# Kernel tuning notes

Measured on AMD Instinct MI355X. Metric: run time of the kernel, lower is better.

Reference implementation:

```python
import jax, jax.numpy as jnp
import numpy as np

N, K, D, E, H, O = 8192, 16, 256, 128, 512, 256


def _mlp(v, W1, W2):
    # nn.Sequential(Linear(no bias), Tanh, Linear(no bias)) with torch [out,in] weights
    return jnp.tanh(v @ W1.T) @ W2.T


def setup_inputs() -> dict:
    key = jax.random.key(0)
    ks = jax.random.split(key, 16)
    def rn(k, shape, s=1.0):
        return jax.random.normal(k, shape, jnp.float32) * s
    return {
        "x": rn(ks[0], (N, D)),
        "neibs": rn(ks[1], (N * K, D)),
        "edge_emb": rn(ks[2], (N * K, E)),
        "mask": jax.random.randint(ks[3], (N, K), 0, 2, jnp.int32),
        "W1x": rn(ks[4], (H, D), 0.02), "W2x": rn(ks[5], (H, H), 0.02),
        "W1n": rn(ks[6], (H, D), 0.02), "W2n": rn(ks[7], (H, H), 0.02),
        "W1e": rn(ks[8], (H, E), 0.02), "W2e": rn(ks[9], (H, H), 0.02),
        "Wfx": rn(ks[10], (O, D), 0.02), "bfx": jnp.zeros((O,), jnp.float32),
        "Wfn": rn(ks[11], (O, D), 0.02), "bfn": jnp.zeros((O,), jnp.float32),
        "Wfe": rn(ks[12], (O, E), 0.02), "bfe": jnp.zeros((O,), jnp.float32),
    }


def reference(x, neibs, edge_emb, mask, W1x, W2x, W1n, W2n, W1e, W2e,
              Wfx, bfx, Wfn, bfn, Wfe, bfe):
    n, d = x.shape
    e = edge_emb.shape[1]
    x_att = _mlp(x, W1x, W2x)                                  # [N,H]
    neib_att = _mlp(neibs, W1n, W2n).reshape(n, -1, H)         # [N,K,H]
    edge_att = _mlp(edge_emb, W1e, W2e).reshape(n, -1, H)      # [N,K,H]

    # node-neighbor attention (scaled by hard-coded sqrt(512))
    ws = jnp.einsum('nkh,nh->nk', neib_att, x_att) / np.sqrt(512.0).astype(np.float32)
    ws = jax.nn.softmax(ws, axis=1)
    agg_neib = jnp.einsum('nk,nkd->nd', ws, neibs.reshape(n, -1, d))
    out = jnp.concatenate([x @ Wfx.T + bfx, agg_neib @ Wfn.T + bfn], axis=1)

    # node-edge attention (unscaled, masked)
    ws2 = jnp.einsum('nkh,nh->nk', edge_att, x_att)
    ws2 = ws2 + (-9999999.0) * mask.astype(x.dtype)
    ws2 = jax.nn.softmax(ws2, axis=1)
    agg_edge = jnp.einsum('nk,nke->ne', ws2, edge_emb.reshape(n, -1, e))
    out = jnp.concatenate([out, agg_edge @ Wfe.T + bfe], axis=1)  # [N,3*O]
    return jax.nn.relu(out)
```

## Files before the change

### kernel.cpp

```cpp
#include <hip/hip_runtime.h>
#include <hip/hip_bf16.h>

typedef __bf16 bf16;
typedef __bf16 bf16x2 __attribute__((ext_vector_type(2)));
typedef __bf16 bf16x4 __attribute__((ext_vector_type(4)));
typedef __bf16 bf16x8 __attribute__((ext_vector_type(8)));
typedef float  f32x4  __attribute__((ext_vector_type(4)));

__device__ __forceinline__ void async16(const bf16* g, bf16* l) {
  __builtin_amdgcn_global_load_lds(
      (__attribute__((address_space(1))) void*)g,
      (__attribute__((address_space(3))) void*)l,
      16, 0, 0);
}

__device__ __forceinline__ void fence_barrier() {
  asm volatile("s_waitcnt vmcnt(0) lgkmcnt(0)" ::: "memory");
  __syncthreads();
}

__device__ __forceinline__ float fast_tanh(float x) {
  float e = __builtin_amdgcn_exp2f(x * 2.88539008177793f);
  return 1.f - 2.f * __builtin_amdgcn_rcpf(e + 1.f);
}

__device__ __forceinline__ int swz(int elem, int row) {
  return elem ^ ((row & 7) << 3);
}

template<int ACT, typename OT>
__global__ __launch_bounds__(256, 4)
void gemm64(const bf16* __restrict__ A, const bf16* __restrict__ W,
            OT* __restrict__ C, int K, int ldc, float alpha,
            const float* __restrict__ bias) {
  __shared__ bf16 As[64 * 64];
  __shared__ bf16 Bs[64 * 64];
  const int tid  = threadIdx.x;
  const int wave = tid >> 6, lane = tid & 63;
  const int wr = wave >> 1, wc = wave & 1;
  const int g = lane >> 4, l4 = lane & 15;

  f32x4 acc[2][2];
#pragma unroll
  for (int i = 0; i < 2; ++i)
#pragma unroll
    for (int j = 0; j < 2; ++j)
      acc[i][j] = (f32x4){0.f, 0.f, 0.f, 0.f};

  const bf16* Abase = A + (size_t)blockIdx.x * 64 * K;
  const bf16* Wbase = W + (size_t)blockIdx.y * 64 * K;

  for (int k0 = 0; k0 < K; k0 += 64) {
#pragma unroll
    for (int i = 0; i < 2; ++i) {
      const int cb  = i * 256 + wave * 64;
      const int c   = cb + lane;
      const int row = c >> 3;
      const int kk  = ((c & 7) ^ (row & 7)) << 3;
      async16(Abase + (size_t)row * K + k0 + kk, &As[cb * 8]);
      async16(Wbase + (size_t)row * K + k0 + kk, &Bs[cb * 8]);
    }
    fence_barrier();
#pragma unroll
    for (int s = 0; s < 2; ++s) {
      const int koff = s * 32 + g * 8;
      bf16x8 af[2], bfr[2];
#pragma unroll
      for (int i = 0; i < 2; ++i) {
        const int ra = wr * 32 + i * 16 + l4;
        af[i] = *(const bf16x8*)&As[ra * 64 + swz(koff, ra)];
      }
#pragma unroll
      for (int j = 0; j < 2; ++j) {
        const int rb = wc * 32 + j * 16 + l4;
        bfr[j] = *(const bf16x8*)&Bs[rb * 64 + swz(koff, rb)];
      }
#pragma unroll
      for (int i = 0; i < 2; ++i)
#pragma unroll
        for (int j = 0; j < 2; ++j)
          acc[i][j] = __builtin_amdgcn_mfma_f32_16x16x32_bf16(af[i], bfr[j], acc[i][j], 0, 0, 0);
    }
    fence_barrier();
  }

  const int rbase = blockIdx.x * 64 + wr * 32;
  const int cbase = blockIdx.y * 64 + wc * 32;
#pragma unroll
  for (int i = 0; i < 2; ++i)
#pragma unroll
    for (int j = 0; j < 2; ++j) {
      const int col = cbase + j * 16 + l4;
      const float bv = bias ? bias[col] : 0.f;
#pragma unroll
      for (int r = 0; r < 4; ++r) {
        const int row = rbase + i * 16 + g * 4 + r;
        float v = acc[i][j][r] * alpha + bv;
        if (ACT == 1) v = fast_tanh(v);
        if (ACT == 2) v = fmaxf(v, 0.f);
        C[(size_t)row * ldc + col] = (OT)v;
      }
    }
}

template<int D>
__global__ __launch_bounds__(256, 2)
void score_agg(const float* __restrict__ A, const bf16* __restrict__ Wb,
               const bf16* __restrict__ y, int ldy, int yoff, float scale,
               const int* __restrict__ mask, bf16* __restrict__ agg) {
  __shared__ bf16 As[64 * D];
  __shared__ bf16 Bs[256 * 64];
  float* sred = (float*)Bs;
  float* wgt  = (float*)Bs + 256;
  const int tid  = threadIdx.x;
  const int wave = tid >> 6, lane = tid & 63;
  const int g = lane >> 4, l4 = lane & 15;
  const int blk = blockIdx.x;

  const float* Ab = A + (size_t)blk * 64 * D;
  constexpr int F4PR = D / 4;
#pragma unroll
  for (int ii = 0; ii < D / 16; ++ii) {
    const int c    = ii * 256 + tid;
    const int row  = c / F4PR;
    const int col4 = (c % F4PR) * 4;
    const float4 v = *(const float4*)(Ab + (size_t)row * D + col4);
    bf16x4 o = {(bf16)v.x, (bf16)v.y, (bf16)v.z, (bf16)v.w};
    *(bf16x4*)&As[row * D + swz(col4, row)] = o;
  }

  float p[4][4];
#pragma unroll
  for (int i = 0; i < 4; ++i)
#pragma unroll
    for (int r = 0; r < 4; ++r) p[i][r] = 0.f;

  fence_barrier();

  for (int j = 0; j < 2; ++j) {
    const bf16* Wj = Wb + (size_t)j * 256 * D;
    f32x4 acc[4][4];
#pragma unroll
    for (int i = 0; i < 4; ++i)
#pragma unroll
      for (int jj = 0; jj < 4; ++jj)
        acc[i][jj] = (f32x4){0.f, 0.f, 0.f, 0.f};

    for (int k0 = 0; k0 < D; k0 += 64) {
#pragma unroll
      for (int i = 0; i < 8; ++i) {
        const int cb  = i * 256 + wave * 64;
        const int c   = cb + lane;
        const int row = c >> 3;
        const int kk  = ((c & 7) ^ (row & 7)) << 3;
        async16(Wj + (size_t)row * D + k0 + kk, &Bs[cb * 8]);
      }
      fence_barrier();
#pragma unroll
      for (int s = 0; s < 2; ++s) {
        const int koff = s * 32 + g * 8;
        bf16x8 af[4], bfr[4];
#pragma unroll
        for (int i = 0; i < 4; ++i) {
          const int ra = i * 16 + l4;
          af[i] = *(const bf16x8*)&As[ra * D + swz(k0 + koff, ra)];
        }
#pragma unroll
        for (int jj = 0; jj < 4; ++jj) {
          const int rb = wave * 64 + jj * 16 + l4;
          bfr[jj] = *(const bf16x8*)&Bs[rb * 64 + swz(koff, rb)];
        }
#pragma unroll
        for (int i = 0; i < 4; ++i)
#pragma unroll
          for (int jj = 0; jj < 4; ++jj)
            acc[i][jj] = __builtin_amdgcn_mfma_f32_16x16x32_bf16(af[i], bfr[jj], acc[i][jj], 0, 0, 0);
      }
      fence_barrier();
    }

#pragma unroll
    for (int i = 0; i < 4; ++i) {
      const size_t yb = (size_t)(blk * 4 + i) * ldy + yoff + j * 256 + wave * 64;
#pragma unroll
      for (int jj = 0; jj < 4; ++jj) {
        const float yv = (float)y[yb + jj * 16 + l4];
        p[i][0] += fast_tanh(acc[i][jj][0]) * yv;
        p[i][1] += fast_tanh(acc[i][jj][1]) * yv;
        p[i][2] += fast_tanh(acc[i][jj][2]) * yv;
        p[i][3] += fast_tanh(acc[i][jj][3]) * yv;
      }
    }
  }

#pragma unroll
  for (int i = 0; i < 4; ++i)
#pragma unroll
    for (int r = 0; r < 4; ++r) {
      float v = p[i][r];
#pragma unroll
      for (int m = 1; m < 16; m <<= 1) v += __shfl_xor(v, m);
      p[i][r] = v;
    }
  if (l4 == 0) {
#pragma unroll
    for (int i = 0; i < 4; ++i)
#pragma unroll
      for (int r = 0; r < 4; ++r)
        sred[wave * 64 + i * 16 + g * 4 + r] = p[i][r];
  }
  __syncthreads();

  if (tid < 64) {
    const int node_g = blk * 4 + (tid >> 4);
    float s = (sred[tid] + sred[64 + tid] + sred[128 + tid] + sred[192 + tid]) * scale;
    if (mask) s -= 9999999.0f * (float)mask[node_g * 16 + (tid & 15)];
    float m = s;
#pragma unroll
    for (int d = 1; d < 16; d <<= 1) m = fmaxf(m, __shfl_xor(m, d));
    float e = __builtin_amdgcn_exp2f((s - m) * 1.44269504088896f);
    float sum = e;
#pragma unroll
    for (int d = 1; d < 16; d <<= 1) sum += __shfl_xor(sum, d);
    wgt[tid] = e / sum;
  }
  __syncthreads();

  constexpr int EPT = D / 64;
  const int n  = tid >> 6;
  const int dl = (tid & 63) * EPT;
  float a[EPT];
#pragma unroll
  for (int e = 0; e < EPT; ++e) a[e] = 0.f;
#pragma unroll
  for (int k = 0; k < 16; ++k) {
    const float w = wgt[n * 16 + k];
    const int rk = n * 16 + k;
    if constexpr (EPT == 4) {
      bf16x4 v = *(const bf16x4*)&As[rk * D + swz(dl, rk)];
      a[0] += w * (float)v[0]; a[1] += w * (float)v[1];
      a[2] += w * (float)v[2]; a[3] += w * (float)v[3];
    } else {
      bf16x2 v = *(const bf16x2*)&As[rk * D + swz(dl, rk)];
      a[0] += w * (float)v[0]; a[1] += w * (float)v[1];
    }
  }
  if constexpr (EPT == 4) {
    bf16x4 o = {(bf16)a[0], (bf16)a[1], (bf16)a[2], (bf16)a[3]};
    *(bf16x4*)&agg[(size_t)(blk * 4 + n) * D + dl] = o;
  } else {
    bf16x2 o = {(bf16)a[0], (bf16)a[1]};
    *(bf16x2*)&agg[(size_t)(blk * 4 + n) * D + dl] = o;
  }
}

struct CvtEnt { const float* s; bf16* d; int n; };
struct CvtArgs { CvtEnt e[8]; };

__global__ void cvt_small(CvtArgs args) {
  const CvtEnt ent = args.e[blockIdx.y];
  const int i = blockIdx.x * 2048 + threadIdx.x * 8;
  if (i < ent.n) {
    const float4 a = *(const float4*)(ent.s + i);
    const float4 c = *(const float4*)(ent.s + i + 4);
    bf16x8 o = { (bf16)a.x, (bf16)a.y, (bf16)a.z, (bf16)a.w,
                 (bf16)c.x, (bf16)c.y, (bf16)c.z, (bf16)c.w };
    *(bf16x8*)(ent.d + i) = o;
  }
}

__global__ void transpose2(const float* __restrict__ s0, bf16* __restrict__ d0,
                           const float* __restrict__ s1, bf16* __restrict__ d1) {
  __shared__ float t[16][17];
  const float* s = blockIdx.z ? s1 : s0;
  bf16* d = blockIdx.z ? d1 : d0;
  const int x0 = blockIdx.x * 16, y0 = blockIdx.y * 16;
  t[threadIdx.y][threadIdx.x] = s[(size_t)(y0 + threadIdx.y) * 512 + x0 + threadIdx.x];
  __syncthreads();
  d[(size_t)(x0 + threadIdx.y) * 512 + (y0 + threadIdx.x)] = (bf16)t[threadIdx.x][threadIdx.y];
}

extern "C" void kernel_launch(void* const* d_in, const int* in_sizes, int n_in,
                              void* d_out, int out_size, void* d_ws, size_t ws_size,
                              hipStream_t stream) {
  const float* x     = (const float*)d_in[0];
  const float* neibs = (const float*)d_in[1];
  const float* edge  = (const float*)d_in[2];
  const int*   mask  = (const int*)d_in[3];
  const float* W1x = (const float*)d_in[4];
  const float* W2x = (const float*)d_in[5];
  const float* W1n = (const float*)d_in[6];
  const float* W2n = (const float*)d_in[7];
  const float* W1e = (const float*)d_in[8];
  const float* W2e = (const float*)d_in[9];
  const float* Wfx = (const float*)d_in[10];
  const float* bfx = (const float*)d_in[11];
  const float* Wfn = (const float*)d_in[12];
  const float* bfn = (const float*)d_in[13];
  const float* Wfe = (const float*)d_in[14];
  const float* bfe = (const float*)d_in[15];
  float* out = (float*)d_out;

  char* wsb = (char*)d_ws;
  const size_t MB = 1024 * 1024;
  bf16* W2nT = (bf16*)(wsb + 0);
  bf16* W2eT = (bf16*)(wsb + 512 * 1024);
  char* wtb  = wsb + 1 * MB;
  bf16* W1xb = (bf16*)(wtb + 0);
  bf16* W2xb = (bf16*)(wtb + 256 * 1024);
  bf16* W1nb = (bf16*)(wtb + 768 * 1024);
  bf16* W1eb = (bf16*)(wtb + 1024 * 1024);
  bf16* Wfxb = (bf16*)(wtb + 1152 * 1024);
  bf16* Wfnb = (bf16*)(wtb + 1280 * 1024);
  bf16* Wfeb = (bf16*)(wtb + 1408 * 1024);
  bf16* xb    = (bf16*)(wsb + 3 * MB);
  bf16* h_x   = (bf16*)(wsb + 7 * MB);
  bf16* x_att = (bf16*)(wsb + 15 * MB);
  bf16* ycat  = (bf16*)(wsb + 23 * MB);
  bf16* aggn  = (bf16*)(wsb + 39 * MB);
  bf16* agge  = (bf16*)(wsb + 43 * MB);

  const float inv_sqrt512 = 0.04419417382415922f;

  CvtArgs ca;
  ca.e[0] = {x,   xb,   2097152};
  ca.e[1] = {W1x, W1xb, 131072};
  ca.e[2] = {W2x, W2xb, 262144};
  ca.e[3] = {W1n, W1nb, 131072};
  ca.e[4] = {W1e, W1eb, 65536};
  ca.e[5] = {Wfx, Wfxb, 65536};
  ca.e[6] = {Wfn, Wfnb, 65536};
  ca.e[7] = {Wfe, Wfeb, 32768};
  cvt_small<<<dim3(1024, 8), 256, 0, stream>>>(ca);

  transpose2<<<dim3(32, 32, 2), dim3(16, 16), 0, stream>>>(W2n, W2nT, W2e, W2eT);

  gemm64<1, bf16><<<dim3(128, 8), 256, 0, stream>>>(xb, W1xb, h_x, 256, 512, 1.f, nullptr);
  gemm64<0, bf16><<<dim3(128, 8), 256, 0, stream>>>(h_x, W2xb, x_att, 512, 512, 1.f, nullptr);
  gemm64<0, bf16><<<dim3(128, 16), 256, 0, stream>>>(x_att, W2nT, ycat, 512, 1024, 1.f, nullptr);

  score_agg<256><<<2048, 256, 0, stream>>>(neibs, W1nb, ycat, 1024, 0, inv_sqrt512, nullptr, aggn);
  score_agg<128><<<2048, 256, 0, stream>>>(edge,  W1eb, ycat, 1024, 512, 1.f, mask, agge);

  gemm64<2, float><<<dim3(128, 4), 256, 0, stream>>>(xb,   Wfxb, out + 0,   256, 768, 1.f, bfx);
  gemm64<2, float><<<dim3(128, 4), 256, 0, stream>>>(aggn, Wfnb, out + 256, 256, 768, 1.f, bfn);
  gemm64<2, float><<<dim3(128, 4), 256, 0, stream>>>(agge, Wfeb, out + 512, 128, 768, 1.f, bfe);
}
```

Before: 395.3 us.

## Double-buffer LDS tiles in gemm64 and score_agg to overlap loads with MFMA

gemm64 now ping-pongs two LDS buffers so the next K-tile's async global-to-LDS copy is issued before the current tile is computed. score_agg splits its weight tile into 32-wide K phases with two buffers and a new swizzle, and prefetches the first tile of the second weight half during the last phase of the first. It also hoists the y loads ahead of the MFMA loop. The aim is to hide global memory latency behind matrix math, at the cost of more LDS in gemm64 (possible occupancy loss) and more barriers per K in score_agg.

```diff
diff --git a/kernel.cpp b/kernel.cpp
--- a/kernel.cpp
+++ b/kernel.cpp
@@ -33,8 +33,8 @@
 void gemm64(const bf16* __restrict__ A, const bf16* __restrict__ W,
             OT* __restrict__ C, int K, int ldc, float alpha,
             const float* __restrict__ bias) {
-  __shared__ bf16 As[64 * 64];
-  __shared__ bf16 Bs[64 * 64];
+  __shared__ bf16 As[2][64 * 64];
+  __shared__ bf16 Bs[2][64 * 64];
   const int tid  = threadIdx.x;
   const int wave = tid >> 6, lane = tid & 63;
   const int wr = wave >> 1, wc = wave & 1;
@@ -50,17 +50,19 @@
   const bf16* Abase = A + (size_t)blockIdx.x * 64 * K;
   const bf16* Wbase = W + (size_t)blockIdx.y * 64 * K;
 
-  for (int k0 = 0; k0 < K; k0 += 64) {
+  auto stage = [&](int buf, int k0) {
 #pragma unroll
     for (int i = 0; i < 2; ++i) {
       const int cb  = i * 256 + wave * 64;
       const int c   = cb + lane;
       const int row = c >> 3;
       const int kk  = ((c & 7) ^ (row & 7)) << 3;
-      async16(Abase + (size_t)row * K + k0 + kk, &As[cb * 8]);
-      async16(Wbase + (size_t)row * K + k0 + kk, &Bs[cb * 8]);
-    }
-    fence_barrier();
+      async16(Abase + (size_t)row * K + k0 + kk, &As[buf][cb * 8]);
+      async16(Wbase + (size_t)row * K + k0 + kk, &Bs[buf][cb * 8]);
+    }
+  };
+
+  auto compute = [&](int buf) {
 #pragma unroll
     for (int s = 0; s < 2; ++s) {
       const int koff = s * 32 + g * 8;
@@ -68,19 +70,29 @@
 #pragma unroll
       for (int i = 0; i < 2; ++i) {
         const int ra = wr * 32 + i * 16 + l4;
-        af[i] = *(const bf16x8*)&As[ra * 64 + swz(koff, ra)];
-      }
-#pragma unroll
-      for (int j = 0; j < 2; ++j) {
-        const int rb = wc * 32 + j * 16 + l4;
-        bfr[j] = *(const bf16x8*)&Bs[rb * 64 + swz(koff, rb)];
+        af[i] = *(const bf16x8*)&As[buf][ra * 64 + swz(koff, ra)];
+      }
+#pragma unroll
+      for (int jf = 0; jf < 2; ++jf) {
+        const int rb = wc * 32 + jf * 16 + l4;
+        bfr[jf] = *(const bf16x8*)&Bs[buf][rb * 64 + swz(koff, rb)];
       }
 #pragma unroll
       for (int i = 0; i < 2; ++i)
 #pragma unroll
-        for (int j = 0; j < 2; ++j)
-          acc[i][j] = __builtin_amdgcn_mfma_f32_16x16x32_bf16(af[i], bfr[j], acc[i][j], 0, 0, 0);
-    }
+        for (int jf = 0; jf < 2; ++jf)
+          acc[i][jf] = __builtin_amdgcn_mfma_f32_16x16x32_bf16(af[i], bfr[jf], acc[i][jf], 0, 0, 0);
+    }
+  };
+
+  stage(0, 0);
+  fence_barrier();
+  for (int k0 = 0; k0 < K; k0 += 128) {
+    if (k0 + 64 < K) stage(1, k0 + 64);
+    compute(0);
+    fence_barrier();
+    if (k0 + 128 < K) stage(0, k0 + 128);
+    compute(1);
     fence_barrier();
   }
 
@@ -109,13 +121,26 @@
                const bf16* __restrict__ y, int ldy, int yoff, float scale,
                const int* __restrict__ mask, bf16* __restrict__ agg) {
   __shared__ bf16 As[64 * D];
-  __shared__ bf16 Bs[256 * 64];
-  float* sred = (float*)Bs;
-  float* wgt  = (float*)Bs + 256;
+  __shared__ bf16 Bs[2][256 * 32];
+  float* sred = (float*)(&Bs[0][0]);
+  float* wgt  = (float*)(&Bs[0][0]) + 256;
   const int tid  = threadIdx.x;
   const int wave = tid >> 6, lane = tid & 63;
   const int g = lane >> 4, l4 = lane & 15;
   const int blk = blockIdx.x;
+
+  auto stageB = [&](const bf16* Wsrc, int k, bf16* B) {
+#pragma unroll
+    for (int i = 0; i < 4; ++i) {
+      const int cb  = i * 256 + wave * 64;
+      const int c   = cb + lane;
+      const int row = c >> 2;
+      const int sl  = (c & 3) ^ ((row >> 1) & 3);
+      async16(Wsrc + (size_t)row * D + k + sl * 8, &B[cb * 8]);
+    }
+  };
+
+  stageB(Wb, 0, Bs[0]);
 
   const float* Ab = A + (size_t)blk * 64 * D;
   constexpr int F4PR = D / 4;
@@ -137,8 +162,19 @@
 
   fence_barrier();
 
+  constexpr int NP = D / 32;
   for (int j = 0; j < 2; ++j) {
     const bf16* Wj = Wb + (size_t)j * 256 * D;
+
+    float yv[4][4];
+#pragma unroll
+    for (int i = 0; i < 4; ++i) {
+      const size_t yb = (size_t)(blk * 4 + i) * ldy + yoff + j * 256 + wave * 64;
+#pragma unroll
+      for (int jj = 0; jj < 4; ++jj)
+        yv[i][jj] = (float)y[yb + jj * 16 + l4];
+    }
+
     f32x4 acc[4][4];
 #pragma unroll
     for (int i = 0; i < 4; ++i)
@@ -146,49 +182,43 @@
       for (int jj = 0; jj < 4; ++jj)
         acc[i][jj] = (f32x4){0.f, 0.f, 0.f, 0.f};
 
-    for (int k0 = 0; k0 < D; k0 += 64) {
-#pragma unroll
-      for (int i = 0; i < 8; ++i) {
-        const int cb  = i * 256 + wave * 64;
-        const int c   = cb + lane;
-        const int row = c >> 3;
-        const int kk  = ((c & 7) ^ (row & 7)) << 3;
-        async16(Wj + (size_t)row * D + k0 + kk, &Bs[cb * 8]);
-      }
+#pragma unroll
+    for (int ph = 0; ph < NP; ++ph) {
+      if (ph + 1 < NP)
+        stageB(Wj, (ph + 1) * 32, Bs[(ph + 1) & 1]);
+      else if (j == 0)
+        stageB(Wb + 256 * D, 0, Bs[(ph + 1) & 1]);
+
+      const int ka = ph * 32 + g * 8;
+      bf16x8 af[4], bfr[4];
+#pragma unroll
+      for (int i = 0; i < 4; ++i) {
+        const int ra = i * 16 + l4;
+        af[i] = *(const bf16x8*)&As[ra * D + swz(ka, ra)];
+      }
+#pragma unroll
+      for (int jj = 0; jj < 4; ++jj) {
+        const int rb = wave * 64 + jj * 16 + l4;
+        const int sl = g ^ ((rb >> 1) & 3);
+        bfr[jj] = *(const bf16x8*)&Bs[ph & 1][rb * 32 + sl * 8];
+      }
+#pragma unroll
+      for (int i = 0; i < 4; ++i)
+#pragma unroll
+        for (int jj = 0; jj < 4; ++jj)
+          acc[i][jj] = __builtin_amdgcn_mfma_f32_16x16x32_bf16(af[i], bfr[jj], acc[i][jj], 0, 0, 0);
       fence_barrier();
-#pragma unroll
-      for (int s = 0; s < 2; ++s) {
-        const int koff = s * 32 + g * 8;
-        bf16x8 af[4], bfr[4];
-#pragma unroll
-        for (int i = 0; i < 4; ++i) {
-          const int ra = i * 16 + l4;
-          af[i] = *(const bf16x8*)&As[ra * D + swz(k0 + koff, ra)];
-        }
-#pragma unroll
-        for (int jj = 0; jj < 4; ++jj) {
-          const int rb = wave * 64 + jj * 16 + l4;
-          bfr[jj] = *(const bf16x8*)&Bs[rb * 64 + swz(koff, rb)];
-        }
-#pragma unroll
-        for (int i = 0; i < 4; ++i)
-#pragma unroll
-          for (int jj = 0; jj < 4; ++jj)
-            acc[i][jj] = __builtin_amdgcn_mfma_f32_16x16x32_bf16(af[i], bfr[jj], acc[i][jj], 0, 0, 0);
-      }
-      fence_barrier();
     }
 
 #pragma unroll
     for (int i = 0; i < 4; ++i) {
-      const size_t yb = (size_t)(blk * 4 + i) * ldy + yoff + j * 256 + wave * 64;
 #pragma unroll
       for (int jj = 0; jj < 4; ++jj) {
-        const float yv = (float)y[yb + jj * 16 + l4];
-        p[i][0] += fast_tanh(acc[i][jj][0]) * yv;
-        p[i][1] += fast_tanh(acc[i][jj][1]) * yv;
-        p[i][2] += fast_tanh(acc[i][jj][2]) * yv;
-        p[i][3] += fast_tanh(acc[i][jj][3]) * yv;
+        const float yvv = yv[i][jj];
+        p[i][0] += fast_tanh(acc[i][jj][0]) * yvv;
+        p[i][1] += fast_tanh(acc[i][jj][1]) * yvv;
+        p[i][2] += fast_tanh(acc[i][jj][2]) * yvv;
+        p[i][3] += fast_tanh(acc[i][jj][3]) * yvv;
       }
     }
   }
```

After: 407.5 us. 3.1% more time.

## Load GEMM operands directly from global into registers, drop LDS staging

Applied to the files above, without the earlier changes.

Both the generic 64x64 GEMM and the score_agg kernel stop staging weight and activation tiles through shared memory with async global-to-LDS loads and barriers. Each lane now reads its MFMA fragments straight from global memory, relying on L1/L2 caching for reuse. This removes the per-tile barriers and frees LDS, which is why score_agg's occupancy hint goes from 2 to 4 blocks. The cost is less data reuse across waves, so there are more global and cache transactions, and the per-lane 16-byte row-strided loads are not coalesced.

```diff
diff --git a/kernel.cpp b/kernel.cpp
--- a/kernel.cpp
+++ b/kernel.cpp
@@ -7,18 +7,6 @@
 typedef __bf16 bf16x8 __attribute__((ext_vector_type(8)));
 typedef float  f32x4  __attribute__((ext_vector_type(4)));
 
-__device__ __forceinline__ void async16(const bf16* g, bf16* l) {
-  __builtin_amdgcn_global_load_lds(
-      (__attribute__((address_space(1))) void*)g,
-      (__attribute__((address_space(3))) void*)l,
-      16, 0, 0);
-}
-
-__device__ __forceinline__ void fence_barrier() {
-  asm volatile("s_waitcnt vmcnt(0) lgkmcnt(0)" ::: "memory");
-  __syncthreads();
-}
-
 __device__ __forceinline__ float fast_tanh(float x) {
   float e = __builtin_amdgcn_exp2f(x * 2.88539008177793f);
   return 1.f - 2.f * __builtin_amdgcn_rcpf(e + 1.f);
@@ -33,8 +21,6 @@
 void gemm64(const bf16* __restrict__ A, const bf16* __restrict__ W,
             OT* __restrict__ C, int K, int ldc, float alpha,
             const float* __restrict__ bias) {
-  __shared__ bf16 As[64 * 64];
-  __shared__ bf16 Bs[64 * 64];
   const int tid  = threadIdx.x;
   const int wave = tid >> 6, lane = tid & 63;
   const int wr = wave >> 1, wc = wave & 1;
@@ -47,41 +33,22 @@
     for (int j = 0; j < 2; ++j)
       acc[i][j] = (f32x4){0.f, 0.f, 0.f, 0.f};
 
-  const bf16* Abase = A + (size_t)blockIdx.x * 64 * K;
-  const bf16* Wbase = W + (size_t)blockIdx.y * 64 * K;
-
-  for (int k0 = 0; k0 < K; k0 += 64) {
-#pragma unroll
-    for (int i = 0; i < 2; ++i) {
-      const int cb  = i * 256 + wave * 64;
-      const int c   = cb + lane;
-      const int row = c >> 3;
-      const int kk  = ((c & 7) ^ (row & 7)) << 3;
-      async16(Abase + (size_t)row * K + k0 + kk, &As[cb * 8]);
-      async16(Wbase + (size_t)row * K + k0 + kk, &Bs[cb * 8]);
-    }
-    fence_barrier();
-#pragma unroll
-    for (int s = 0; s < 2; ++s) {
-      const int koff = s * 32 + g * 8;
-      bf16x8 af[2], bfr[2];
-#pragma unroll
-      for (int i = 0; i < 2; ++i) {
-        const int ra = wr * 32 + i * 16 + l4;
-        af[i] = *(const bf16x8*)&As[ra * 64 + swz(koff, ra)];
-      }
-#pragma unroll
-      for (int j = 0; j < 2; ++j) {
-        const int rb = wc * 32 + j * 16 + l4;
-        bfr[j] = *(const bf16x8*)&Bs[rb * 64 + swz(koff, rb)];
-      }
-#pragma unroll
-      for (int i = 0; i < 2; ++i)
-#pragma unroll
-        for (int j = 0; j < 2; ++j)
-          acc[i][j] = __builtin_amdgcn_mfma_f32_16x16x32_bf16(af[i], bfr[j], acc[i][j], 0, 0, 0);
-    }
-    fence_barrier();
+  const bf16* Ap = A + ((size_t)blockIdx.x * 64 + wr * 32 + l4) * K;
+  const bf16* Wp = W + ((size_t)blockIdx.y * 64 + wc * 32 + l4) * K;
+
+#pragma unroll 4
+  for (int k0 = 0; k0 < K; k0 += 32) {
+    const int ko = k0 + g * 8;
+    bf16x8 af[2], bfr[2];
+    af[0]  = *(const bf16x8*)&Ap[ko];
+    af[1]  = *(const bf16x8*)&Ap[(size_t)16 * K + ko];
+    bfr[0] = *(const bf16x8*)&Wp[ko];
+    bfr[1] = *(const bf16x8*)&Wp[(size_t)16 * K + ko];
+#pragma unroll
+    for (int i = 0; i < 2; ++i)
+#pragma unroll
+      for (int j = 0; j < 2; ++j)
+        acc[i][j] = __builtin_amdgcn_mfma_f32_16x16x32_bf16(af[i], bfr[j], acc[i][j], 0, 0, 0);
   }
 
   const int rbase = blockIdx.x * 64 + wr * 32;
@@ -104,14 +71,13 @@
 }
 
 template<int D>
-__global__ __launch_bounds__(256, 2)
+__global__ __launch_bounds__(256, 4)
 void score_agg(const float* __restrict__ A, const bf16* __restrict__ Wb,
                const bf16* __restrict__ y, int ldy, int yoff, float scale,
                const int* __restrict__ mask, bf16* __restrict__ agg) {
   __shared__ bf16 As[64 * D];
-  __shared__ bf16 Bs[256 * 64];
-  float* sred = (float*)Bs;
-  float* wgt  = (float*)Bs + 256;
+  __shared__ float sred[256];
+  __shared__ float wgt[64];
   const int tid  = threadIdx.x;
   const int wave = tid >> 6, lane = tid & 63;
   const int g = lane >> 4, l4 = lane & 15;
@@ -135,8 +101,9 @@
 #pragma unroll
     for (int r = 0; r < 4; ++r) p[i][r] = 0.f;
 
-  fence_barrier();
-
+  __syncthreads();
+
+  constexpr int NP = D / 32;
   for (int j = 0; j < 2; ++j) {
     const bf16* Wj = Wb + (size_t)j * 256 * D;
     f32x4 acc[4][4];
@@ -146,37 +113,25 @@
       for (int jj = 0; jj < 4; ++jj)
         acc[i][jj] = (f32x4){0.f, 0.f, 0.f, 0.f};
 
-    for (int k0 = 0; k0 < D; k0 += 64) {
-#pragma unroll
-      for (int i = 0; i < 8; ++i) {
-        const int cb  = i * 256 + wave * 64;
-        const int c   = cb + lane;
-        const int row = c >> 3;
-        const int kk  = ((c & 7) ^ (row & 7)) << 3;
-        async16(Wj + (size_t)row * D + k0 + kk, &Bs[cb * 8]);
+#pragma unroll
+    for (int ph = 0; ph < NP; ++ph) {
+      const int ka = ph * 32 + g * 8;
+      bf16x8 af[4], bfr[4];
+#pragma unroll
+      for (int i = 0; i < 4; ++i) {
+        const int ra = i * 16 + l4;
+        af[i] = *(const bf16x8*)&As[ra * D + swz(ka, ra)];
       }
-      fence_barrier();
-#pragma unroll
-      for (int s = 0; s < 2; ++s) {
-        const int koff = s * 32 + g * 8;
-        bf16x8 af[4], bfr[4];
-#pragma unroll
-        for (int i = 0; i < 4; ++i) {
-          const int ra = i * 16 + l4;
-          af[i] = *(const bf16x8*)&As[ra * D + swz(k0 + koff, ra)];
-        }
-#pragma unroll
-        for (int jj = 0; jj < 4; ++jj) {
-          const int rb = wave * 64 + jj * 16 + l4;
-          bfr[jj] = *(const bf16x8*)&Bs[rb * 64 + swz(koff, rb)];
-        }
-#pragma unroll
-        for (int i = 0; i < 4; ++i)
-#pragma unroll
-          for (int jj = 0; jj < 4; ++jj)
-            acc[i][jj] = __builtin_amdgcn_mfma_f32_16x16x32_bf16(af[i], bfr[jj], acc[i][jj], 0, 0, 0);
+#pragma unroll
+      for (int jj = 0; jj < 4; ++jj) {
+        const int rb = wave * 64 + jj * 16 + l4;
+        bfr[jj] = *(const bf16x8*)&Wj[(size_t)rb * D + ka];
       }
-      fence_barrier();
+#pragma unroll
+      for (int i = 0; i < 4; ++i)
+#pragma unroll
+        for (int jj = 0; jj < 4; ++jj)
+          acc[i][jj] = __builtin_amdgcn_mfma_f32_16x16x32_bf16(af[i], bfr[jj], acc[i][jj], 0, 0, 0);
     }
 
 #pragma unroll
```

Result: slower. 726.8 us (+83.9%).

## Double score_agg tile to 128 rows with 512-thread blocks and K32 B staging

Applied to the files above, without the earlier changes.

The score_agg kernel now processes 128 neighbor rows (8 nodes) per block with 8 waves in a 2x4 grid, so each staged W1 tile is reused across twice as many rows. The B tile shrinks to 256x32 with a new XOR swizzle, and the first tile is prefetched before the A conversion so its load overlaps that work. The intent is to cut repeated weight traffic and the number of barriers per row. The cost is twice the A shared-memory footprint (64KB for D=256), which limits how many blocks fit per CU, plus more barrier phases, each covering a smaller K step.

```diff
diff --git a/kernel.cpp b/kernel.cpp
--- a/kernel.cpp
+++ b/kernel.cpp
@@ -104,24 +104,38 @@
 }
 
 template<int D>
-__global__ __launch_bounds__(256, 2)
+__global__ __launch_bounds__(512, 4)
 void score_agg(const float* __restrict__ A, const bf16* __restrict__ Wb,
                const bf16* __restrict__ y, int ldy, int yoff, float scale,
                const int* __restrict__ mask, bf16* __restrict__ agg) {
-  __shared__ bf16 As[64 * D];
-  __shared__ bf16 Bs[256 * 64];
+  __shared__ bf16 As[128 * D];
+  __shared__ bf16 Bs[256 * 32];
   float* sred = (float*)Bs;
-  float* wgt  = (float*)Bs + 256;
+  float* wgt  = (float*)Bs + 512;
   const int tid  = threadIdx.x;
   const int wave = tid >> 6, lane = tid & 63;
+  const int wr = wave >> 2, wc = wave & 3;
   const int g = lane >> 4, l4 = lane & 15;
   const int blk = blockIdx.x;
 
-  const float* Ab = A + (size_t)blk * 64 * D;
+  auto stageB = [&](const bf16* Wsrc, int k) {
+#pragma unroll
+    for (int i = 0; i < 2; ++i) {
+      const int cb  = i * 512 + wave * 64;
+      const int c   = cb + lane;
+      const int row = c >> 2;
+      const int sl  = (c & 3) ^ ((row >> 1) & 3);
+      async16(Wsrc + (size_t)row * D + k + sl * 8, &Bs[cb * 8]);
+    }
+  };
+
+  stageB(Wb, 0);
+
+  const float* Ab = A + (size_t)blk * 128 * D;
   constexpr int F4PR = D / 4;
 #pragma unroll
   for (int ii = 0; ii < D / 16; ++ii) {
-    const int c    = ii * 256 + tid;
+    const int c    = ii * 512 + tid;
     const int row  = c / F4PR;
     const int col4 = (c % F4PR) * 4;
     const float4 v = *(const float4*)(Ab + (size_t)row * D + col4);
@@ -137,8 +151,8 @@
 
   fence_barrier();
 
+  constexpr int NP = D / 32;
   for (int j = 0; j < 2; ++j) {
-    const bf16* Wj = Wb + (size_t)j * 256 * D;
     f32x4 acc[4][4];
 #pragma unroll
     for (int i = 0; i < 4; ++i)
@@ -146,42 +160,40 @@
       for (int jj = 0; jj < 4; ++jj)
         acc[i][jj] = (f32x4){0.f, 0.f, 0.f, 0.f};
 
-    for (int k0 = 0; k0 < D; k0 += 64) {
-#pragma unroll
-      for (int i = 0; i < 8; ++i) {
-        const int cb  = i * 256 + wave * 64;
-        const int c   = cb + lane;
-        const int row = c >> 3;
-        const int kk  = ((c & 7) ^ (row & 7)) << 3;
-        async16(Wj + (size_t)row * D + k0 + kk, &Bs[cb * 8]);
-      }
+#pragma unroll
+    for (int ph = 0; ph < NP; ++ph) {
+      const int ka = ph * 32 + g * 8;
+      bf16x8 af[4], bfr[4];
+#pragma unroll
+      for (int i = 0; i < 4; ++i) {
+        const int ra = wr * 64 + i * 16 + l4;
+        af[i] = *(const bf16x8*)&As[ra * D + swz(ka, ra)];
+      }
+#pragma unroll
+      for (int jj = 0; jj < 4; ++jj) {
+        const int rb = wc * 64 + jj * 16 + l4;
+        const int sl = g ^ ((rb >> 1) & 3);
+        bfr[jj] = *(const bf16x8*)&Bs[rb * 32 + sl * 8];
+      }
+#pragma unroll
+      for (int i = 0; i < 4; ++i)
+#pragma unroll
+        for (int jj = 0; jj < 4; ++jj)
+          acc[i][jj] = __builtin_amdgcn_mfma_f32_16x16x32_bf16(af[i], bfr[jj], acc[i][jj], 0, 0, 0);
+
       fence_barrier();
-#pragma unroll
-      for (int s = 0; s < 2; ++s) {
-        const int koff = s * 32 + g * 8;
-        bf16x8 af[4], bfr[4];
-#pragma unroll
-        for (int i = 0; i < 4; ++i) {
-          const int ra = i * 16 + l4;
-          af[i] = *(const bf16x8*)&As[ra * D + swz(k0 + koff, ra)];
-        }
-#pragma unroll
-        for (int jj = 0; jj < 4; ++jj) {
-          const int rb = wave * 64 + jj * 16 + l4;
-          bfr[jj] = *(const bf16x8*)&Bs[rb * 64 + swz(koff, rb)];
-        }
-#pragma unroll
-        for (int i = 0; i < 4; ++i)
-#pragma unroll
-          for (int jj = 0; jj < 4; ++jj)
-            acc[i][jj] = __builtin_amdgcn_mfma_f32_16x16x32_bf16(af[i], bfr[jj], acc[i][jj], 0, 0, 0);
-      }
-      fence_barrier();
+      if (ph + 1 < NP) {
+        stageB(Wb + (size_t)j * 256 * D, (ph + 1) * 32);
+        fence_barrier();
+      } else if (j == 0) {
+        stageB(Wb + (size_t)256 * D, 0);
+        fence_barrier();
+      }
     }
 
 #pragma unroll
     for (int i = 0; i < 4; ++i) {
-      const size_t yb = (size_t)(blk * 4 + i) * ldy + yoff + j * 256 + wave * 64;
+      const size_t yb = (size_t)(blk * 8 + wr * 4 + i) * ldy + yoff + j * 256 + wc * 64;
 #pragma unroll
       for (int jj = 0; jj < 4; ++jj) {
         const float yv = (float)y[yb + jj * 16 + l4];
@@ -207,13 +219,13 @@
     for (int i = 0; i < 4; ++i)
 #pragma unroll
       for (int r = 0; r < 4; ++r)
-        sred[wave * 64 + i * 16 + g * 4 + r] = p[i][r];
+        sred[wc * 128 + wr * 64 + i * 16 + g * 4 + r] = p[i][r];
   }
   __syncthreads();
 
-  if (tid < 64) {
-    const int node_g = blk * 4 + (tid >> 4);
-    float s = (sred[tid] + sred[64 + tid] + sred[128 + tid] + sred[192 + tid]) * scale;
+  if (tid < 128) {
+    const int node_g = blk * 8 + (tid >> 4);
+    float s = (sred[tid] + sred[128 + tid] + sred[256 + tid] + sred[384 + tid]) * scale;
     if (mask) s -= 9999999.0f * (float)mask[node_g * 16 + (tid & 15)];
     float m = s;
 #pragma unroll
@@ -247,10 +259,10 @@
   }
   if constexpr (EPT == 4) {
     bf16x4 o = {(bf16)a[0], (bf16)a[1], (bf16)a[2], (bf16)a[3]};
-    *(bf16x4*)&agg[(size_t)(blk * 4 + n) * D + dl] = o;
+    *(bf16x4*)&agg[(size_t)(blk * 8 + n) * D + dl] = o;
   } else {
     bf16x2 o = {(bf16)a[0], (bf16)a[1]};
-    *(bf16x2*)&agg[(size_t)(blk * 4 + n) * D + dl] = o;
+    *(bf16x2*)&agg[(size_t)(blk * 8 + n) * D + dl] = o;
   }
 }
 
@@ -339,8 +351,8 @@
   gemm64<0, bf16><<<dim3(128, 8), 256, 0, stream>>>(h_x, W2xb, x_att, 512, 512, 1.f, nullptr);
   gemm64<0, bf16><<<dim3(128, 16), 256, 0, stream>>>(x_att, W2nT, ycat, 512, 1024, 1.f, nullptr);
 
-  score_agg<256><<<2048, 256, 0, stream>>>(neibs, W1nb, ycat, 1024, 0, inv_sqrt512, nullptr, aggn);
-  score_agg<128><<<2048, 256, 0, stream>>>(edge,  W1eb, ycat, 1024, 512, 1.f, mask, agge);
+  score_agg<256><<<1024, 512, 0, stream>>>(neibs, W1nb, ycat, 1024, 0, inv_sqrt512, nullptr, aggn);
+  score_agg<128><<<1024, 512, 0, stream>>>(edge,  W1eb, ycat, 1024, 512, 1.f, mask, agge);
 
   gemm64<2, float><<<dim3(128, 4), 256, 0, stream>>>(xb,   Wfxb, out + 0,   256, 768, 1.f, bfx);
   gemm64<2, float><<<dim3(128, 4), 256, 0, stream>>>(aggn, Wfnb, out + 256, 256, 768, 1.f, bfn);
```

Result: slower. 467.5 us (+18.3%).
